# Optimization experiments

Measured on AMD Instinct MI355X. Metric: run time of the kernel, lower is better.

Reference implementation:

```python
import jax, jax.numpy as jnp
import numpy as np

B, T, V, D, H = 128, 512, 32000, 1024, 2048


def _rnn_layer(x, lengths, W_ih, W_hh, b):
    """Masked (ragged) Elman RNN layer.
    x: [B,T,Din], lengths: [B] int. Returns (outputs [B,T,H], final hidden [B,H]).
    Hidden state is frozen once t >= length (packed-sequence semantics)."""
    Bx, Tx, _ = x.shape
    Hh = W_hh.shape[0]
    # Precompute input projection for all timesteps in one big GEMM.
    xp = jnp.einsum('btd,dh->bth', x, W_ih) + b  # [B,T,H]

    def step(h, inp):
        xt, t = inp  # xt: [B,H]
        hn = jnp.tanh(xt + h @ W_hh)
        h = jnp.where((t < lengths)[:, None], hn, h)
        return h, h

    h0 = jnp.zeros((Bx, Hh), x.dtype)
    hT, hs = jax.lax.scan(step, h0, (jnp.swapaxes(xp, 0, 1), jnp.arange(Tx)))
    return jnp.swapaxes(hs, 0, 1), hT


def setup_inputs() -> dict:
    key = jax.random.key(0)
    ks = jax.random.split(key, 9)
    tokens = jax.random.randint(ks[0], (B, T), 0, V, dtype=jnp.int64)
    lengths = jax.random.randint(ks[1], (B,), 1, T + 1, dtype=jnp.int32)
    emb = jax.random.normal(ks[2], (V, D), dtype=jnp.float32) * 0.02
    s_in = 1.0 / np.sqrt(D)
    s_h = 1.0 / np.sqrt(H)
    W_ih0 = jax.random.normal(ks[3], (D, H), dtype=jnp.float32) * s_in
    W_hh0 = jax.random.normal(ks[4], (H, H), dtype=jnp.float32) * s_h
    b0 = jnp.zeros((H,), jnp.float32)
    W_ih1 = jax.random.normal(ks[5], (H, H), dtype=jnp.float32) * s_h
    W_hh1 = jax.random.normal(ks[6], (H, H), dtype=jnp.float32) * s_h
    b1 = jnp.zeros((H,), jnp.float32)
    return {"tokens": tokens, "lengths": lengths, "emb": emb,
            "W_ih0": W_ih0, "W_hh0": W_hh0, "b0": b0,
            "W_ih1": W_ih1, "W_hh1": W_hh1, "b1": b1}


def reference(tokens, lengths, emb, W_ih0, W_hh0, b0, W_ih1, W_hh1, b1):
    x = emb[tokens]                                   # [B,T,D]
    x, _ = _rnn_layer(x, lengths, W_ih0, W_hh0, b0)   # layer 0 outputs [B,T,H]
    _, h = _rnn_layer(x, lengths, W_ih1, W_hh1, b1)   # layer 1 final hidden
    return h                                          # [B,H]
```

## Files before the change

### kernel.cpp

```cpp
#include <hip/hip_runtime.h>
#include <stdint.h>
#include <stddef.h>

#define Bq 128
#define Tq 512
#define Vq 32000
#define Dq 1024
#define Hq 2048
#define BH (Bq * Hq)

typedef __attribute__((ext_vector_type(8))) _Float16 h8;
typedef __attribute__((ext_vector_type(4))) float f4;
typedef unsigned long long ull;

__device__ __forceinline__ float h2f(unsigned short u){
  _Float16 h; __builtin_memcpy(&h, &u, 2); return (float)h;
}
__device__ __forceinline__ unsigned short f2h(float f){
  _Float16 h = (_Float16)f; unsigned short u; __builtin_memcpy(&u, &h, 2); return u;
}
__device__ __forceinline__ float fast_tanh(float x){
  float e = __expf(2.0f * x);
  return 1.0f - 2.0f / (e + 1.0f);
}
__device__ __forceinline__ ull pack4h(float a, float b, float c, float d){
  return (ull)f2h(a) | ((ull)f2h(b) << 16) | ((ull)f2h(c) << 32) | ((ull)f2h(d) << 48);
}

__device__ __forceinline__ ull ld_q(const ull* p){
  return __hip_atomic_load(p, __ATOMIC_RELAXED, __HIP_MEMORY_SCOPE_AGENT);
}
__device__ __forceinline__ void st_q(ull* p, ull v){
  __hip_atomic_store(p, v, __ATOMIC_RELAXED, __HIP_MEMORY_SCOPE_AGENT);
}
__device__ __forceinline__ unsigned ld_u(const unsigned* p){
  return __hip_atomic_load(p, __ATOMIC_RELAXED, __HIP_MEMORY_SCOPE_AGENT);
}
__device__ __forceinline__ unsigned add_u(unsigned* p, unsigned v){
  return __hip_atomic_fetch_add(p, v, __ATOMIC_RELAXED, __HIP_MEMORY_SCOPE_AGENT);
}

template<int SC>
__device__ __forceinline__ h8 ald16(const void* p){
  h8 d;
  if constexpr (SC == 1)
    asm volatile("global_load_dwordx4 %0, %1, off sc0" : "=v"(d) : "v"(p));
  else
    asm volatile("global_load_dwordx4 %0, %1, off sc1" : "=v"(d) : "v"(p));
  return d;
}
template<int N>
__device__ __forceinline__ void vwait(){
  asm volatile("s_waitcnt vmcnt(%0)" :: "i"(N) : "memory");
  __builtin_amdgcn_sched_barrier(0);
}


__global__ void transpose_cast(const float* __restrict__ in, unsigned short* __restrict__ out, int K, int N){
  __shared__ float tile[32][33];
  int n0 = blockIdx.x * 32, k0 = blockIdx.y * 32;
  int tx = threadIdx.x, ty = threadIdx.y;
  #pragma unroll
  for (int i = 0; i < 32; i += 8)
    tile[ty + i][tx] = in[(size_t)(k0 + ty + i) * N + n0 + tx];
  __syncthreads();
  #pragma unroll
  for (int i = 0; i < 32; i += 8)
    out[(size_t)(n0 + ty + i) * K + k0 + tx] = f2h(tile[tx][ty + i]);
}

__global__ void h2f_out(const unsigned short* __restrict__ in, float* __restrict__ out, int n){
  int i = blockIdx.x * blockDim.x + threadIdx.x;
  if (i < n) out[i] = h2f(in[i]);
}


template<int MT, int NT, int KF, int MODE>
__device__ __forceinline__ void mmX(f4 (&acc)[MT][NT],
    const char* const (&ap)[MT], const char* Wl,
    const int (&bb)[NT], const int (&swz)[NT])
{
  h8 ab[4][MT];
  auto lda2 = [&](int kf, int mt) -> h8 {
    const float4* p = (const float4*)(ap[mt] + kf * 128);
    float4 x = p[0], y = p[1];
    h8 h;
    h[0] = (_Float16)x.x; h[1] = (_Float16)x.y; h[2] = (_Float16)x.z; h[3] = (_Float16)x.w;
    h[4] = (_Float16)y.x; h[5] = (_Float16)y.y; h[6] = (_Float16)y.z; h[7] = (_Float16)y.w;
    return h;
  };
  #pragma unroll
  for (int kf = 0; kf < 4 && kf < KF; ++kf)
    #pragma unroll
    for (int mt = 0; mt < MT; ++mt){
      if constexpr (MODE == 1) ab[kf][mt] = ald16<2>(ap[mt] + kf * 64);
      else if constexpr (MODE == 3) ab[kf][mt] = ald16<1>(ap[mt] + kf * 64);
      else ab[kf][mt] = lda2(kf, mt);
    }
  #pragma unroll
  for (int kf = 0; kf < KF; ++kf){
    if constexpr (MODE != 2){
      const int rem = KF - 1 - kf;
      if (rem >= 3) vwait<3*MT>();
      else if (rem == 2) vwait<2*MT>();
      else if (rem == 1) vwait<MT>();
      else vwait<0>();
    }
    h8 b[NT];
    #pragma unroll
    for (int nt = 0; nt < NT; ++nt)
      b[nt] = *(const h8*)(Wl + ((bb[nt] + kf * 64) ^ swz[nt]));
    #pragma unroll
    for (int mt = 0; mt < MT; ++mt)
      #pragma unroll
      for (int nt = 0; nt < NT; ++nt)
        acc[mt][nt] = __builtin_amdgcn_mfma_f32_16x16x32_f16(ab[kf & 3][mt], b[nt], acc[mt][nt], 0, 0, 0);
    if (kf + 4 < KF){
      #pragma unroll
      for (int mt = 0; mt < MT; ++mt){
        if constexpr (MODE == 1) ab[kf & 3][mt] = ald16<2>(ap[mt] + (kf + 4) * 64);
        else if constexpr (MODE == 3) ab[kf & 3][mt] = ald16<1>(ap[mt] + (kf + 4) * 64);
        else ab[kf & 3][mt] = lda2(kf + 4, mt);
      }
    }
  }
}


__device__ __forceinline__ void sbar(unsigned* sc, unsigned n){
  __syncthreads();
  if (threadIdx.x == 0){
    add_u(sc, 1u);
    while (ld_u(sc) < n) __builtin_amdgcn_s_sleep(1);
    asm volatile("" ::: "memory");
  }
  __syncthreads();
}

__device__ __forceinline__ void gbar(unsigned* arr, unsigned* gc, int sub, int it){
  __syncthreads();
  if (threadIdx.x == 0){
    add_u(arr, 1u);
    if (sub == 0){
      while (ld_u(arr) < 32u * (unsigned)(it + 1)) __builtin_amdgcn_s_sleep(1);
      add_u(gc, 1u);
    }
    while (ld_u(gc) < 8u * (unsigned)(it + 1)) __builtin_amdgcn_s_sleep(1);
    asm volatile("" ::: "memory");
  }
  __syncthreads();
}


__global__ __launch_bounds__(512, 2) void rnn4(
    const float* __restrict__ emb,
    const int* __restrict__ tokens,
    const unsigned short* __restrict__ Wih0T,
    const unsigned short* __restrict__ Whh0T,
    const unsigned short* __restrict__ Wih1T,
    const unsigned short* __restrict__ Whh1T,
    const float* __restrict__ b0,
    const float* __restrict__ b1,
    unsigned short* __restrict__ h0,
    unsigned short* __restrict__ h1,
    unsigned short* __restrict__ P0,
    unsigned short* __restrict__ P1a,
    unsigned short* __restrict__ P1b,
    unsigned short* __restrict__ stg,
    const int* __restrict__ lengths,
    unsigned* __restrict__ zp)
{
  extern __shared__ char lds[];
  char* Wl = lds;
  char* zone = lds + 131072;
  __shared__ int s_grp, s_sub, s_coop;

  const int tid = threadIdx.x, l = tid & 63, w = tid >> 6;
  const int mw = w & 1, kw = w >> 1;
  const int fr = l & 15, q = l >> 4;

  if (tid == 0){
    unsigned x;
    asm volatile("s_getreg_b32 %0, hwreg(HW_REG_XCC_ID)" : "=s"(x));
    x &= 7u;
    unsigned mysub = add_u(&zp[x], 1u);
    add_u(&zp[33], 1u);
    while (ld_u(&zp[33]) < 256u) __builtin_amdgcn_s_sleep(1);
    unsigned cnt[8]; int coop = 1;
    #pragma unroll
    for (int i = 0; i < 8; ++i){ cnt[i] = ld_u(&zp[i]); if (cnt[i] != 32u) coop = 0; }
    int g = (int)x, s = (int)mysub;
    if (mysub >= 32u){
      unsigned j = add_u(&zp[34], 1u);
      for (int xx = 0; xx < 8; ++xx){
        unsigned have = (cnt[xx] < 32u) ? (32u - cnt[xx]) : 0u;
        if (j < have){ g = xx; s = (int)(cnt[xx] + j); break; }
        j -= have;
      }
    }
    s_grp = g; s_sub = s; s_coop = coop;
  }
  __syncthreads();
  const int grp = s_grp, sub = s_sub;
  const bool coop = (s_coop != 0);
  unsigned* gc   = zp + 32;
  unsigned* arr  = zp + 256 + grp * 64;
  unsigned* sctr = zp + 256 + grp * 64 + 32;

  int role = -1, tile = 0;
  if (grp == 0){ role = 0; tile = sub; }
  else if (grp <= 2){ role = 1; tile = (grp - 1) * 32 + sub; }
  else if (grp <= 4){ role = 2; tile = (grp - 3) * 32 + sub; }
  else if (grp <= 6){ role = 3; tile = (grp - 5) * 32 + sub; }

  const int kh = (role == 2) ? (tile & 1) : 0;
  const int c0 = (role == 0) ? tile * 64 : (role == 2) ? (tile >> 1) * 64 : tile * 32;

  if (role >= 0){
    const unsigned short* src; int NC, KC, srcK, kofs;
    if (role == 0){ src = Wih0T; NC = 64; KC = 1024; srcK = 1024; kofs = 0; }
    else if (role == 2){ src = Wih1T; NC = 64; KC = 1024; srcK = 2048; kofs = kh * 1024; }
    else { src = (role == 1) ? Whh0T : Whh1T; NC = 32; KC = 2048; srcK = 2048; kofs = 0; }
    int nch = NC * (KC / 8);
    for (int i2 = tid; i2 < nch; i2 += 512){
      int c = i2 / (KC / 8), kg = i2 % (KC / 8);
      uint4 v = *(const uint4*)(src + (size_t)(c0 + c) * srcK + kofs + kg * 8);
      int byte = (c * KC + kg * 8) * 2 ^ ((c & 31) << 4);
      *(uint4*)(Wl + byte) = v;
    }
  }
  __syncthreads();

  bool w64 = false;
  if (grp == 0) w64 = ((tokens[1] | tokens[3] | tokens[5] | tokens[7]) == 0);

  const int rIP = tid >> 3;
  float bias8[8] = {0,0,0,0,0,0,0,0};
  if (role == 0){
    #pragma unroll
    for (int j = 0; j < 8; ++j) bias8[j] = b0[c0 + (tid & 7) * 8 + j];
  } else if (role == 2 && kh == 0){
    #pragma unroll
    for (int j = 0; j < 8; ++j) bias8[j] = b1[c0 + (tid & 7) * 8 + j];
  }
  int lenRow[2] = {0, 0};
  float hpz[2][4] = {{0,0,0,0},{0,0,0,0}};
  if (role == 1 || role == 3){
    lenRow[0] = lengths[rIP];
    lenRow[1] = lengths[64 + rIP];
  }

  unsigned stct = 0;
  for (int it = 0; it < 515; ++it){
    const unsigned short* stga = nullptr;

    if (coop){
      if (grp == 0){
        if (it <= 511){
          unsigned short* sd = stg;
          int gt = sub * 512 + tid;
          int row = gt >> 7;
          int c8 = (gt & 127) * 8;
          long tix = (long)row * Tq + it;
          int tok = w64 ? tokens[2 * tix] : tokens[tix];
          const float* sf = emb + (size_t)tok * Dq + c8;
          float4 f0 = *(const float4*)sf;
          float4 f1 = *(const float4*)(sf + 4);
          h8 hv;
          hv[0] = (_Float16)f0.x; hv[1] = (_Float16)f0.y; hv[2] = (_Float16)f0.z; hv[3] = (_Float16)f0.w;
          hv[4] = (_Float16)f1.x; hv[5] = (_Float16)f1.y; hv[6] = (_Float16)f1.z; hv[7] = (_Float16)f1.w;
          *(h8*)(sd + row * 1024 + c8) = hv;
          ++stct;
          sbar(sctr, 32u * stct);
          stga = sd;
        }
      } else if (grp <= 6){
        const int lo = (grp <= 2) ? 1 : (grp <= 4) ? 2 : 3;
        if (it >= lo && it <= lo + 511){
          const unsigned short* hsrc = ((grp <= 4) ? h0 : h1) + (it & 1) * BH;
          unsigned short* sd = stg + (size_t)grp * BH;
          int gt = sub * 512 + tid;
          const char* sb = (const char*)hsrc;
          char* db = (char*)sd;
          h8 v0 = ald16<2>(sb + (size_t)gt * 32);
          h8 v1 = ald16<2>(sb + (size_t)gt * 32 + 16);
          vwait<0>();
          *(h8*)(db + (size_t)gt * 32) = v0;
          *(h8*)(db + (size_t)gt * 32 + 16) = v1;
          ++stct;
          sbar(sctr, 32u * stct);
          stga = sd;
        }
      }
    }

    if (role == 0 || role == 2){
      const int t = (role == 0) ? it : it - 2;
      if (t >= 0 && t <= 511){
        int bb[4], swz[4];
        #pragma unroll
        for (int nt = 0; nt < 4; ++nt){
          int cl = nt * 16 + fr;
          bb[nt] = (cl * 1024 + kw * 256 + q * 8) * 2;
          swz[nt] = (cl & 31) << 4;
        }
        const char* ap[4];
        f4 acc[4][4] = {};
        if (role == 0){
          if (coop){
            #pragma unroll
            for (int mt = 0; mt < 4; ++mt){
              int row = mw * 64 + mt * 16 + fr;
              ap[mt] = (const char*)(stga + (size_t)row * 1024 + kw * 256 + q * 8);
            }
            mmX<4, 4, 8, 3>(acc, ap, Wl, bb, swz);
          } else {
            #pragma unroll
            for (int mt = 0; mt < 4; ++mt){
              int row = mw * 64 + mt * 16 + fr;
              long idx = (long)row * Tq + t;
              int tok = w64 ? tokens[2 * idx] : tokens[idx];
              ap[mt] = (const char*)(emb + (size_t)tok * Dq) + kw * 1024 + q * 32;
            }
            mmX<4, 4, 8, 2>(acc, ap, Wl, bb, swz);
          }
        } else {
          const unsigned short* asrc = coop ? stga : (h0 + (it & 1) * BH);
          #pragma unroll
          for (int mt = 0; mt < 4; ++mt){
            int row = mw * 64 + mt * 16 + fr;
            ap[mt] = (const char*)(asrc + (size_t)row * Hq + kh * 1024 + kw * 256 + q * 8);
          }
          if (coop) mmX<4, 4, 8, 3>(acc, ap, Wl, bb, swz);
          else      mmX<4, 4, 8, 1>(acc, ap, Wl, bb, swz);
        }

        unsigned short* dst = ((role == 0) ? P0 : (kh == 0 ? P1a : P1b)) + (t & 1) * BH;
        #pragma unroll
        for (int mwr = 0; mwr < 2; ++mwr){
          __syncthreads();
          if (mw == mwr && kw > 0){
            #pragma unroll
            for (int mt = 0; mt < 4; ++mt)
              #pragma unroll
              for (int nt = 0; nt < 4; ++nt){
                ushort4 u = { f2h(acc[mt][nt][0]), f2h(acc[mt][nt][1]),
                              f2h(acc[mt][nt][2]), f2h(acc[mt][nt][3]) };
                *(ushort4*)(zone + (kw - 1) * 8192 + (mt * 4 + nt) * 512 + l * 8) = u;
              }
          }
          __syncthreads();
          if (mw == mwr && kw == 0){
            #pragma unroll
            for (int mt = 0; mt < 4; ++mt)
              #pragma unroll
              for (int nt = 0; nt < 4; ++nt){
                #pragma unroll
                for (int j = 0; j < 3; ++j){
                  ushort4 u = *(ushort4*)(zone + j * 8192 + (mt * 4 + nt) * 512 + l * 8);
                  acc[mt][nt][0] += h2f(u.x); acc[mt][nt][1] += h2f(u.y);
                  acc[mt][nt][2] += h2f(u.z); acc[mt][nt][3] += h2f(u.w);
                }
              }
          }
          __syncthreads();
          if (mw == mwr && kw == 0){
            float* szw = (float*)zone;
            #pragma unroll
            for (int mt = 0; mt < 4; ++mt)
              #pragma unroll
              for (int nt = 0; nt < 4; ++nt)
                #pragma unroll
                for (int r = 0; r < 4; ++r)
                  szw[(mt * 16 + q * 4 + r) * 64 + nt * 16 + fr] = acc[mt][nt][r];
          }
          __syncthreads();
          {
            const float* sz = (const float*)zone;
            int cL = (tid & 7) * 8;
            float v[8];
            #pragma unroll
            for (int j = 0; j < 8; ++j) v[j] = sz[rIP * 64 + cL + j] + bias8[j];
            size_t o = (size_t)(mwr * 64 + rIP) * Hq + (c0 + cL);
            st_q((ull*)(dst + o),     pack4h(v[0], v[1], v[2], v[3]));
            st_q((ull*)(dst + o) + 1, pack4h(v[4], v[5], v[6], v[7]));
          }
        }
      }
    } else if (role == 1 || role == 3){
      const int t = (role == 1) ? it - 1 : it - 3;
      if (t >= 0 && t <= 511){
        int bb[2], swz[2];
        #pragma unroll
        for (int nt = 0; nt < 2; ++nt){
          int cl = nt * 16 + fr;
          bb[nt] = (cl * 2048 + kw * 512 + q * 8) * 2;
          swz[nt] = (cl & 31) << 4;
        }
        unsigned short* hbuf = (role == 1) ? h0 : h1;
        const unsigned short* asrc = coop ? stga : (hbuf + (it & 1) * BH);
        const char* ap[4];
        #pragma unroll
        for (int mt = 0; mt < 4; ++mt){
          int row = mw * 64 + mt * 16 + fr;
          ap[mt] = (const char*)(asrc + (size_t)row * Hq + kw * 512 + q * 8);
        }
        f4 acc[4][2] = {};
        if (coop) mmX<4, 2, 16, 3>(acc, ap, Wl, bb, swz);
        else      mmX<4, 2, 16, 1>(acc, ap, Wl, bb, swz);

        const unsigned short* Pa = ((role == 1) ? P0 : P1a) + (t & 1) * BH;
        const unsigned short* Pb = (role == 3) ? (P1b + (t & 1) * BH) : nullptr;
        unsigned short* hdst = hbuf + (t & 1) * BH;
        #pragma unroll
        for (int mwr = 0; mwr < 2; ++mwr){
          __syncthreads();
          if (mw == mwr && kw > 0){
            #pragma unroll
            for (int mt = 0; mt < 4; ++mt)
              #pragma unroll
              for (int nt = 0; nt < 2; ++nt){
                ushort4 u = { f2h(acc[mt][nt][0]), f2h(acc[mt][nt][1]),
                              f2h(acc[mt][nt][2]), f2h(acc[mt][nt][3]) };
                *(ushort4*)(zone + (kw - 1) * 8192 + (mt * 2 + nt) * 512 + l * 8) = u;
              }
          }
          __syncthreads();
          if (mw == mwr && kw == 0){
            #pragma unroll
            for (int mt = 0; mt < 4; ++mt)
              #pragma unroll
              for (int nt = 0; nt < 2; ++nt){
                #pragma unroll
                for (int j = 0; j < 3; ++j){
                  ushort4 u = *(ushort4*)(zone + j * 8192 + (mt * 2 + nt) * 512 + l * 8);
                  acc[mt][nt][0] += h2f(u.x); acc[mt][nt][1] += h2f(u.y);
                  acc[mt][nt][2] += h2f(u.z); acc[mt][nt][3] += h2f(u.w);
                }
              }
          }
          __syncthreads();
          if (mw == mwr && kw == 0){
            float* szw = (float*)zone;
            #pragma unroll
            for (int mt = 0; mt < 4; ++mt)
              #pragma unroll
              for (int nt = 0; nt < 2; ++nt)
                #pragma unroll
                for (int r = 0; r < 4; ++r)
                  szw[(mt * 16 + q * 4 + r) * 32 + nt * 16 + fr] = acc[mt][nt][r];
          }
          __syncthreads();
          {
            const float* sz = (const float*)zone;
            int cL = (tid & 7) * 4;
            size_t o = (size_t)(mwr * 64 + rIP) * Hq + (c0 + cL);
            float v[4];
            #pragma unroll
            for (int j = 0; j < 4; ++j) v[j] = sz[rIP * 32 + cL + j];
            ull pa = ld_q((const ull*)(Pa + o));
            #pragma unroll
            for (int j = 0; j < 4; ++j) v[j] += h2f((unsigned short)(pa >> (16 * j)));
            if (role == 3){
              ull pb = ld_q((const ull*)(Pb + o));
              #pragma unroll
              for (int j = 0; j < 4; ++j) v[j] += h2f((unsigned short)(pb >> (16 * j)));
            }
            const int len = lenRow[mwr];
            float ho[4];
            #pragma unroll
            for (int j = 0; j < 4; ++j){
              float hn = fast_tanh(v[j]);
              float x = (t < len) ? hn : hpz[mwr][j];
              hpz[mwr][j] = x;
              ho[j] = x;
            }
            st_q((ull*)(hdst + o), pack4h(ho[0], ho[1], ho[2], ho[3]));
          }
        }
      }
    }
    if (it < 514) gbar(arr, gc, sub, it);
  }
}


extern "C" void kernel_launch(void* const* d_in, const int* in_sizes, int n_in,
                              void* d_out, int out_size, void* d_ws, size_t ws_size,
                              hipStream_t stream)
{
  (void)in_sizes; (void)n_in; (void)out_size; (void)ws_size;
  const int*   tokens  = (const int*)d_in[0];
  const int*   lengths = (const int*)d_in[1];
  const float* emb     = (const float*)d_in[2];
  const float* Wih0    = (const float*)d_in[3];
  const float* Whh0    = (const float*)d_in[4];
  const float* b0      = (const float*)d_in[5];
  const float* Wih1    = (const float*)d_in[6];
  const float* Whh1    = (const float*)d_in[7];
  const float* b1      = (const float*)d_in[8];

  char* ws = (char*)d_ws;
  size_t off = 0;
  auto alloc = [&](size_t bytes)->char*{
    char* p = ws + off; off += (bytes + 255) & ~(size_t)255; return p;
  };
  unsigned short* WTih0 = (unsigned short*)alloc((size_t)Hq * Dq * 2);
  unsigned short* WThh0 = (unsigned short*)alloc((size_t)Hq * Hq * 2);
  unsigned short* WTih1 = (unsigned short*)alloc((size_t)Hq * Hq * 2);
  unsigned short* WThh1 = (unsigned short*)alloc((size_t)Hq * Hq * 2);
  unsigned short* h0b   = (unsigned short*)alloc((size_t)2 * BH * 2);
  unsigned short* h1b   = (unsigned short*)alloc((size_t)2 * BH * 2);
  unsigned short* P0b   = (unsigned short*)alloc((size_t)2 * BH * 2);
  unsigned short* P1ab  = (unsigned short*)alloc((size_t)2 * BH * 2);
  unsigned short* P1bb  = (unsigned short*)alloc((size_t)2 * BH * 2);
  unsigned short* stgb  = (unsigned short*)alloc((size_t)8 * BH * 2);
  unsigned*       zp    = (unsigned*)alloc(4096);

  transpose_cast<<<dim3(Hq / 32, Dq / 32), dim3(32, 8), 0, stream>>>(Wih0, WTih0, Dq, Hq);
  transpose_cast<<<dim3(Hq / 32, Hq / 32), dim3(32, 8), 0, stream>>>(Whh0, WThh0, Hq, Hq);
  transpose_cast<<<dim3(Hq / 32, Hq / 32), dim3(32, 8), 0, stream>>>(Wih1, WTih1, Hq, Hq);
  transpose_cast<<<dim3(Hq / 32, Hq / 32), dim3(32, 8), 0, stream>>>(Whh1, WThh1, Hq, Hq);

  hipMemsetAsync(h0b, 0, (size_t)2 * BH * 2, stream);
  hipMemsetAsync(h1b, 0, (size_t)2 * BH * 2, stream);
  hipMemsetAsync(zp, 0, 4096, stream);

  hipFuncSetAttribute((const void*)rnn4, hipFuncAttributeMaxDynamicSharedMemorySize, 155648);
  rnn4<<<256, 512, 155648, stream>>>(emb, tokens, WTih0, WThh0, WTih1, WThh1,
                                     b0, b1, h0b, h1b, P0b, P1ab, P1bb, stgb,
                                     lengths, zp);

  h2f_out<<<(BH + 255) / 256, 256, 0, stream>>>(h1b + BH, (float*)d_out, BH);
}
```

Measured before the change: 14.58 ms.

## Deepen A-operand prefetch, hoist projection loads, and pad LDS reduction tiles

The A-fragment register ring in the MFMA loop grows from 4 to 8 stages for the global-load modes, with the vmcnt waits extended to match, so more load latency is hidden behind MFMAs. The recurrent roles now load the precomputed input-projection values before the matmul rather than after it, overlapping those global loads with compute. The LDS staging rows for the cross-warp reduction are padded (64→68 and 32→36 floats) to reduce bank conflicts, and the per-group barrier counter moves to a different offset. The cost is more registers for the deeper prefetch, which may lower occupancy. The moved counter could also collide with arrival slots if more than 16 are in use.

```diff
diff --git a/kernel.cpp b/kernel.cpp
--- a/kernel.cpp
+++ b/kernel.cpp
@@ -80,7 +80,9 @@
     const char* const (&ap)[MT], const char* Wl,
     const int (&bb)[NT], const int (&swz)[NT])
 {
-  h8 ab[4][MT];
+  constexpr int DP  = (MODE == 2) ? 4 : 8;
+  constexpr int MSK = DP - 1;
+  h8 ab[DP][MT];
   auto lda2 = [&](int kf, int mt) -> h8 {
     const float4* p = (const float4*)(ap[mt] + kf * 128);
     float4 x = p[0], y = p[1];
@@ -89,8 +91,9 @@
     h[4] = (_Float16)y.x; h[5] = (_Float16)y.y; h[6] = (_Float16)y.z; h[7] = (_Float16)y.w;
     return h;
   };
+  constexpr int PRE = (KF < DP) ? KF : DP;
   #pragma unroll
-  for (int kf = 0; kf < 4 && kf < KF; ++kf)
+  for (int kf = 0; kf < PRE; ++kf)
     #pragma unroll
     for (int mt = 0; mt < MT; ++mt){
       if constexpr (MODE == 1) ab[kf][mt] = ald16<2>(ap[mt] + kf * 64);
@@ -101,9 +104,14 @@
   for (int kf = 0; kf < KF; ++kf){
     if constexpr (MODE != 2){
       const int rem = KF - 1 - kf;
-      if (rem >= 3) vwait<3*MT>();
-      else if (rem == 2) vwait<2*MT>();
-      else if (rem == 1) vwait<MT>();
+      const int rr = rem < (DP - 1) ? rem : (DP - 1);
+      if (rr == 7) vwait<7*MT>();
+      else if (rr == 6) vwait<6*MT>();
+      else if (rr == 5) vwait<5*MT>();
+      else if (rr == 4) vwait<4*MT>();
+      else if (rr == 3) vwait<3*MT>();
+      else if (rr == 2) vwait<2*MT>();
+      else if (rr == 1) vwait<1*MT>();
       else vwait<0>();
     }
     h8 b[NT];
@@ -114,13 +122,13 @@
     for (int mt = 0; mt < MT; ++mt)
       #pragma unroll
       for (int nt = 0; nt < NT; ++nt)
-        acc[mt][nt] = __builtin_amdgcn_mfma_f32_16x16x32_f16(ab[kf & 3][mt], b[nt], acc[mt][nt], 0, 0, 0);
-    if (kf + 4 < KF){
+        acc[mt][nt] = __builtin_amdgcn_mfma_f32_16x16x32_f16(ab[kf & MSK][mt], b[nt], acc[mt][nt], 0, 0, 0);
+    if (kf + DP < KF){
       #pragma unroll
       for (int mt = 0; mt < MT; ++mt){
-        if constexpr (MODE == 1) ab[kf & 3][mt] = ald16<2>(ap[mt] + (kf + 4) * 64);
-        else if constexpr (MODE == 3) ab[kf & 3][mt] = ald16<1>(ap[mt] + (kf + 4) * 64);
-        else ab[kf & 3][mt] = lda2(kf + 4, mt);
+        if constexpr (MODE == 1) ab[kf & MSK][mt] = ald16<2>(ap[mt] + (kf + DP) * 64);
+        else if constexpr (MODE == 3) ab[kf & MSK][mt] = ald16<1>(ap[mt] + (kf + DP) * 64);
+        else ab[kf & MSK][mt] = lda2(kf + DP, mt);
       }
     }
   }
@@ -205,7 +213,7 @@
   const bool coop = (s_coop != 0);
   unsigned* gc   = zp + 32;
   unsigned* arr  = zp + 256 + grp * 64;
-  unsigned* sctr = zp + 256 + grp * 64 + 32;
+  unsigned* sctr = zp + 256 + grp * 64 + 16;
 
   int role = -1, tile = 0;
   if (grp == 0){ role = 0; tile = sub; }
@@ -372,7 +380,7 @@
               for (int nt = 0; nt < 4; ++nt)
                 #pragma unroll
                 for (int r = 0; r < 4; ++r)
-                  szw[(mt * 16 + q * 4 + r) * 64 + nt * 16 + fr] = acc[mt][nt][r];
+                  szw[(mt * 16 + q * 4 + r) * 68 + nt * 16 + fr] = acc[mt][nt][r];
           }
           __syncthreads();
           {
@@ -380,7 +388,7 @@
             int cL = (tid & 7) * 8;
             float v[8];
             #pragma unroll
-            for (int j = 0; j < 8; ++j) v[j] = sz[rIP * 64 + cL + j] + bias8[j];
+            for (int j = 0; j < 8; ++j) v[j] = sz[rIP * 68 + cL + j] + bias8[j];
             size_t o = (size_t)(mwr * 64 + rIP) * Hq + (c0 + cL);
             st_q((ull*)(dst + o),     pack4h(v[0], v[1], v[2], v[3]));
             st_q((ull*)(dst + o) + 1, pack4h(v[4], v[5], v[6], v[7]));
@@ -390,6 +398,16 @@
     } else if (role == 1 || role == 3){
       const int t = (role == 1) ? it - 1 : it - 3;
       if (t >= 0 && t <= 511){
+        const unsigned short* Pa = ((role == 1) ? P0 : P1a) + (t & 1) * BH;
+        const unsigned short* Pb = (role == 3) ? (P1b + (t & 1) * BH) : nullptr;
+        ull paPre[2], pbPre[2] = {0, 0};
+        #pragma unroll
+        for (int mwr = 0; mwr < 2; ++mwr){
+          size_t o = (size_t)(mwr * 64 + rIP) * Hq + (c0 + (tid & 7) * 4);
+          paPre[mwr] = ld_q((const ull*)(Pa + o));
+          if (role == 3) pbPre[mwr] = ld_q((const ull*)(Pb + o));
+        }
+
         int bb[2], swz[2];
         #pragma unroll
         for (int nt = 0; nt < 2; ++nt){
@@ -409,8 +427,6 @@
         if (coop) mmX<4, 2, 16, 3>(acc, ap, Wl, bb, swz);
         else      mmX<4, 2, 16, 1>(acc, ap, Wl, bb, swz);
 
-        const unsigned short* Pa = ((role == 1) ? P0 : P1a) + (t & 1) * BH;
-        const unsigned short* Pb = (role == 3) ? (P1b + (t & 1) * BH) : nullptr;
         unsigned short* hdst = hbuf + (t & 1) * BH;
         #pragma unroll
         for (int mwr = 0; mwr < 2; ++mwr){
@@ -448,7 +464,7 @@
               for (int nt = 0; nt < 2; ++nt)
                 #pragma unroll
                 for (int r = 0; r < 4; ++r)
-                  szw[(mt * 16 + q * 4 + r) * 32 + nt * 16 + fr] = acc[mt][nt][r];
+                  szw[(mt * 16 + q * 4 + r) * 36 + nt * 16 + fr] = acc[mt][nt][r];
           }
           __syncthreads();
           {
@@ -457,12 +473,12 @@
             size_t o = (size_t)(mwr * 64 + rIP) * Hq + (c0 + cL);
             float v[4];
             #pragma unroll
-            for (int j = 0; j < 4; ++j) v[j] = sz[rIP * 32 + cL + j];
-            ull pa = ld_q((const ull*)(Pa + o));
+            for (int j = 0; j < 4; ++j) v[j] = sz[rIP * 36 + cL + j];
+            ull pa = paPre[mwr];
             #pragma unroll
             for (int j = 0; j < 4; ++j) v[j] += h2f((unsigned short)(pa >> (16 * j)));
             if (role == 3){
-              ull pb = ld_q((const ull*)(Pb + o));
+              ull pb = pbPre[mwr];
               #pragma unroll
               for (int j = 0; j < 4; ++j) v[j] += h2f((unsigned short)(pb >> (16 * j)));
             }
```

After: 18.85 ms. 29.3% more time.
